# Performance work log

Measured on AMD Instinct MI355X. Metric: run time of the kernel, lower is better.

The kernel has to match this reference:

```python
import jax, jax.numpy as jnp
import numpy as np

N, E, G = 50000, 800000, 256
NODE_IN, EDGE_IN, H, L, RO, OUT = 64, 16, 128, 3, 128, 2
EPS = 1e-5


def _ln(x, g, b):
    m = jnp.mean(x, axis=-1, keepdims=True)
    v = jnp.mean((x - m) ** 2, axis=-1, keepdims=True)
    return (x - m) * jax.lax.rsqrt(v + EPS) * g + b


def setup_inputs() -> dict:
    key = jax.random.key(0)
    ks = iter(jax.random.split(key, 40))
    w = lambda *s: jax.random.normal(next(ks), s, dtype=jnp.float32) * 0.05
    inp = {
        "x": jax.random.normal(next(ks), (N, NODE_IN), dtype=jnp.float32),
        "edge_attr": jax.random.normal(next(ks), (E, EDGE_IN), dtype=jnp.float32),
        "edge_index": jax.random.randint(next(ks), (2, E), 0, N, dtype=jnp.int32),
        "batch": jnp.sort(jax.random.randint(next(ks), (N,), 0, G, dtype=jnp.int32)),
        # encoders + input norms
        "node_enc_w": w(NODE_IN, H), "node_enc_b": jnp.zeros((H,), jnp.float32),
        "edge_enc_w": w(EDGE_IN, H), "edge_enc_b": jnp.zeros((H,), jnp.float32),
        "node_ln_g": jnp.ones((H,), jnp.float32), "node_ln_b": jnp.zeros((H,), jnp.float32),
        "edge_ln_g": jnp.ones((H,), jnp.float32), "edge_ln_b": jnp.zeros((H,), jnp.float32),
        # per-layer stacked params [L, ...]
        "msg_w1": w(L, 2 * H, H), "msg_b1": jnp.zeros((L, H), jnp.float32),
        "msg_w2": w(L, H, H), "msg_b2": jnp.zeros((L, H), jnp.float32),
        "gate_w": w(L, 2 * H, H), "gate_b": jnp.zeros((L, H), jnp.float32),
        "res_w1": w(L, 2 * H, H), "res_b1": jnp.zeros((L, H), jnp.float32),
        "res_w2": w(L, H, H), "res_b2": jnp.zeros((L, H), jnp.float32),
        "ln_g": jnp.ones((L, H), jnp.float32), "ln_b": jnp.zeros((L, H), jnp.float32),
        # readout MLP
        "ro_w1": w(H, RO), "ro_b1": jnp.zeros((RO,), jnp.float32),
        "ro_w2": w(RO, OUT), "ro_b2": jnp.zeros((OUT,), jnp.float32),
    }
    return inp


def reference(x, edge_attr, edge_index, batch,
              node_enc_w, node_enc_b, edge_enc_w, edge_enc_b,
              node_ln_g, node_ln_b, edge_ln_g, edge_ln_b,
              msg_w1, msg_b1, msg_w2, msg_b2, gate_w, gate_b,
              res_w1, res_b1, res_w2, res_b2, ln_g, ln_b,
              ro_w1, ro_b1, ro_w2, ro_b2):
    src, dst = edge_index[0], edge_index[1]
    h = _ln(x @ node_enc_w + node_enc_b, node_ln_g, node_ln_b)        # [N,H]
    e = _ln(edge_attr @ edge_enc_w + edge_enc_b, edge_ln_g, edge_ln_b)  # [E,H]
    for l in range(L):
        cat = jnp.concatenate([h[src], e], axis=-1)                   # [E,2H]
        gate = jax.nn.sigmoid(cat @ gate_w[l] + gate_b[l])
        msg = jax.nn.relu(cat @ msg_w1[l] + msg_b1[l]) @ msg_w2[l] + msg_b2[l]
        agg = jax.ops.segment_sum(gate * msg, dst, num_segments=N)    # scatter-add
        comb = jnp.concatenate([h, agg], axis=-1)                     # [N,2H]
        res = jax.nn.relu(comb @ res_w1[l] + res_b1[l]) @ res_w2[l] + res_b2[l]
        h = _ln(h + res, ln_g[l], ln_b[l])
    # global mean pool over graphs
    sums = jax.ops.segment_sum(h, batch, num_segments=G)              # [G,H]
    cnt = jax.ops.segment_sum(jnp.ones((h.shape[0],), h.dtype), batch, num_segments=G)
    g = sums / jnp.maximum(cnt, 1.0)[:, None]
    return jax.nn.relu(g @ ro_w1 + ro_b1) @ ro_w2 + ro_b2             # [G,OUT]
```

## Files before the change

### kernel.cpp

```cpp
#include <hip/hip_runtime.h>
#include <math.h>

#define NN 50000
#define NE 800000
#define NG 256
#define H 128
#define NIN 64
#define EIN 16
#define NL 3
#define LEPS 1e-5f

typedef short bf16x8 __attribute__((ext_vector_type(8)));
typedef float f32x4 __attribute__((ext_vector_type(4)));
typedef float f32x16 __attribute__((ext_vector_type(16)));

__device__ __forceinline__ short bf16rne(float x) {
  unsigned u = __float_as_uint(x);
  unsigned r = u + 0x7fff + ((u >> 16) & 1);
  return (short)(r >> 16);
}

__device__ __forceinline__ float wsum(float v) {
#pragma unroll
  for (int m = 1; m < 64; m <<= 1) v += __shfl_xor(v, m, 64);
  return v;
}

__device__ __forceinline__ float lds_f32(const short* p) {
  short2 s = *(const short2*)p;
  return __uint_as_float((unsigned)(unsigned short)s.x |
                         ((unsigned)(unsigned short)s.y << 16));
}

__global__ __launch_bounds__(256) void k_count(const int* __restrict__ eidx,
                                               unsigned* __restrict__ cnt) {
  int t = blockIdx.x * 256 + threadIdx.x;
  if (t < NE) atomicAdd(&cnt[eidx[NE + t]], 1u);
}

__global__ __launch_bounds__(1024) void k_scan(const unsigned* __restrict__ cnt,
                                               unsigned* __restrict__ rowptr) {
  __shared__ unsigned part[16];
  __shared__ unsigned carry_s;
  const int tid = threadIdx.x, lane = tid & 63, wid = tid >> 6;
  if (tid == 0) carry_s = 0;
  __syncthreads();
  for (int base = 0; base < NN; base += 1024) {
    int i = base + tid;
    unsigned v = (i < NN) ? cnt[i] : 0u;
    unsigned incl = v;
#pragma unroll
    for (int off = 1; off < 64; off <<= 1) {
      unsigned t = __shfl_up(incl, off, 64);
      if (lane >= off) incl += t;
    }
    if (lane == 63) part[wid] = incl;
    __syncthreads();
    if (tid == 0) {
      unsigned s = 0;
#pragma unroll
      for (int w = 0; w < 16; w++) { unsigned t = part[w]; part[w] = s; s += t; }
    }
    __syncthreads();
    unsigned carry = carry_s;
    if (i < NN) rowptr[i] = carry + part[wid] + incl - v;
    __syncthreads();
    if (tid == 1023) carry_s = carry + part[15] + incl;
    __syncthreads();
  }
}

__global__ __launch_bounds__(256) void k_fold(
    const float* __restrict__ gate_w, const float* __restrict__ msg_w1,
    const float* __restrict__ e_enc_w, const float* __restrict__ e_enc_b,
    const float* __restrict__ e_ln_g, const float* __restrict__ e_ln_b,
    short* __restrict__ w2e, float* __restrict__ c123,
    float* __restrict__ stats) {
  const int S_W2E = 3 * 4096;
  const int S_C = S_W2E + 3 * 768;
  const int S_ST = S_C + 290;
  int tid = blockIdx.x * 256 + threadIdx.x;
  if (tid >= S_ST) return;
  if (tid < S_W2E) {
    int l = tid / 4096, e = tid % 4096;
    int t = e >> 9, lane = (e >> 3) & 63, j = e & 7;
    int k = (lane >> 5) * 8 + j;
    int n = t * 32 + (lane & 31);
    float s = 0.f;
    for (int m = 0; m < 128; m++) {
      float w = (n < 128) ? gate_w[((size_t)l * 256 + 128 + m) * 128 + n]
                          : msg_w1[((size_t)l * 256 + 128 + m) * 128 + (n - 128)];
      s += e_enc_w[k * 128 + m] * e_ln_g[m] * w;
    }
    w2e[tid] = bf16rne(s);
  } else if (tid < S_C) {
    int e = tid - S_W2E;
    int l = e / 768, r = e % 768, which = r / 256, n = r % 256;
    float s = 0.f;
    for (int m = 0; m < 128; m++) {
      float w = (n < 128) ? gate_w[((size_t)l * 256 + 128 + m) * 128 + n]
                          : msg_w1[((size_t)l * 256 + 128 + m) * 128 + (n - 128)];
      float f = (which == 0) ? e_enc_b[m] * e_ln_g[m]
              : (which == 1) ? e_ln_g[m] : e_ln_b[m];
      s += f * w;
    }
    c123[e] = s;
  } else {
    int e = tid - S_C;
    if (e < 256) {
      int i = e >> 4, j = e & 15;
      float s = 0.f;
      for (int n = 0; n < 128; n++)
        s += e_enc_w[i * 128 + n] * e_enc_w[j * 128 + n];
      stats[e] = s;
    } else if (e < 272) {
      int k = e - 256;
      float s = 0.f;
      for (int n = 0; n < 128; n++) s += e_enc_w[k * 128 + n];
      stats[e] = s;
    } else if (e < 288) {
      int k = e - 272;
      float s = 0.f;
      for (int n = 0; n < 128; n++) s += e_enc_w[k * 128 + n] * e_enc_b[n];
      stats[e] = s;
    } else if (e == 288) {
      float s = 0.f;
      for (int n = 0; n < 128; n++) s += e_enc_b[n] * e_enc_b[n];
      stats[e] = s;
    } else {
      float s = 0.f;
      for (int n = 0; n < 128; n++) s += e_enc_b[n];
      stats[e] = s;
    }
  }
}

__global__ __launch_bounds__(256) void k_scatter(
    const int* __restrict__ eidx, const float* __restrict__ ea,
    const unsigned* __restrict__ rowptr, unsigned* __restrict__ cursor,
    const float* __restrict__ stats,
    int* __restrict__ src_s, int* __restrict__ dst_s,
    short* __restrict__ ea_bf, float2* __restrict__ rsmu) {
  __shared__ float S[290];
  for (int i = threadIdx.x; i < 290; i += 256) S[i] = stats[i];
  __syncthreads();
  int t = blockIdx.x * 256 + threadIdx.x;
  int s = eidx[t], d = eidx[NE + t];
  unsigned pos = rowptr[d] + atomicAdd(&cursor[d], 1u);
  src_s[pos] = s;
  dst_s[pos] = d;
  const float4* er = (const float4*)(ea + (size_t)t * EIN);
  float4 q0 = er[0], q1 = er[1], q2 = er[2], q3 = er[3];
  float e16[16];
  e16[0]=q0.x; e16[1]=q0.y; e16[2]=q0.z; e16[3]=q0.w;
  e16[4]=q1.x; e16[5]=q1.y; e16[6]=q1.z; e16[7]=q1.w;
  e16[8]=q2.x; e16[9]=q2.y; e16[10]=q2.z; e16[11]=q2.w;
  e16[12]=q3.x; e16[13]=q3.y; e16[14]=q3.z; e16[15]=q3.w;
  short tmp[16];
#pragma unroll
  for (int j = 0; j < 16; j++) tmp[j] = bf16rne(e16[j]);
  short* dstp = ea_bf + (size_t)pos * EIN;
  *(bf16x8*)dstp = *(bf16x8*)tmp;
  *(bf16x8*)(dstp + 8) = *(bf16x8*)(tmp + 8);
  float s1 = S[289], s2 = S[288];
#pragma unroll
  for (int k = 0; k < 16; k++) {
    s1 = fmaf(e16[k], S[256 + k], s1);
    s2 = fmaf(2.f * e16[k], S[272 + k], s2);
  }
#pragma unroll
  for (int i = 0; i < 16; i++) {
    float mi = 0.f;
#pragma unroll
    for (int j = 0; j < 16; j++) mi = fmaf(S[i * 16 + j], e16[j], mi);
    s2 = fmaf(e16[i], mi, s2);
  }
  float mu = s1 * (1.f / 128.f);
  float var = s2 * (1.f / 128.f) - mu * mu;
  float rs = rsqrtf(var + LEPS);
  rsmu[pos] = make_float2(rs, mu);
}

__global__ __launch_bounds__(256) void k_convert_w(
    const float* __restrict__ gate_w, const float* __restrict__ msg_w1,
    const float* __restrict__ msg_w2, const float* __restrict__ e_enc_w,
    const float* __restrict__ res_w1, const float* __restrict__ res_w2,
    short* __restrict__ bgh, short* __restrict__ bm2, short* __restrict__ benc,
    short* __restrict__ brs1, short* __restrict__ brs2) {
  const int S_BGH = 3 * 65536;
  const int S_BM2 = S_BGH + 3 * 16384;
  const int S_BEN = S_BM2 + 2048;
  const int S_BR1 = S_BEN + 3 * 32768;
  const int S_BR2 = S_BR1 + 3 * 16384;
  int tid = blockIdx.x * 256 + threadIdx.x;
  if (tid >= S_BR2) return;
  if (tid < S_BGH) {
    int l = tid / 65536, e = tid % 65536;
    int f = e >> 9, lane = (e >> 3) & 63, j = e & 7;
    int nt = f >> 4, ks = f & 15;
    int k = ks * 16 + (lane >> 5) * 8 + j;
    int n = nt * 32 + (lane & 31);
    float v = (n < 128) ? gate_w[((size_t)l * 256 + k) * 128 + n]
                        : msg_w1[((size_t)l * 256 + k) * 128 + (n - 128)];
    bgh[tid] = bf16rne(v);
  } else if (tid < S_BM2) {
    int e0 = tid - S_BGH;
    int l = e0 / 16384, e = e0 % 16384;
    int f = e >> 9, lane = (e >> 3) & 63, j = e & 7;
    int nt = f >> 3, ks = f & 7;
    int k = ks * 16 + (lane >> 5) * 8 + j;
    int n = nt * 32 + (lane & 31);
    bm2[e0] = bf16rne(msg_w2[((size_t)l * 128 + k) * 128 + n]);
  } else if (tid < S_BEN) {
    int e = tid - S_BM2;
    int t = e >> 9, lane = (e >> 3) & 63, j = e & 7;
    int k = (lane >> 5) * 8 + j;
    int n = t * 32 + (lane & 31);
    benc[e] = bf16rne(e_enc_w[k * H + n]);
  } else if (tid < S_BR1) {
    int e0 = tid - S_BEN;
    int l = e0 / 32768, e = e0 % 32768;
    int f = e >> 9, lane = (e >> 3) & 63, j = e & 7;
    int nt = f >> 3, ks = f & 7;
    int k = ks * 32 + (lane >> 4) * 8 + j;
    int n = nt * 16 + (lane & 15);
    brs1[e0] = bf16rne(res_w1[((size_t)l * 256 + k) * 128 + n]);
  } else {
    int e0 = tid - S_BR1;
    int l = e0 / 16384, e = e0 % 16384;
    int f = e >> 9, lane = (e >> 3) & 63, j = e & 7;
    int nt = f >> 2, ks = f & 3;
    int k = ks * 32 + (lane >> 4) * 8 + j;
    int n = nt * 16 + (lane & 15);
    brs2[e0] = bf16rne(res_w2[((size_t)l * 128 + k) * 128 + n]);
  }
}

__global__ __launch_bounds__(256) void k_node_encode(
    const float* __restrict__ x, const float* __restrict__ W,
    const float* __restrict__ bias,
    const float* __restrict__ lng, const float* __restrict__ lnb,
    float* __restrict__ h, short* __restrict__ h_bf) {
  __shared__ float xs[4][8 * NIN];
  const int wave = threadIdx.x >> 6, lane = threadIdx.x & 63;
  const int n0 = (blockIdx.x * 4 + wave) * 8;
  float* xt = xs[wave];
  for (int i = lane; i < 8 * NIN; i += 64) {
    int idx = n0 * NIN + i;
    xt[i] = (idx < NN * NIN) ? x[idx] : 0.f;
  }
  __syncthreads();
  const int c0 = lane, c1 = lane + 64;
  float a0[8], a1[8];
#pragma unroll
  for (int j = 0; j < 8; j++) { a0[j] = 0.f; a1[j] = 0.f; }
  for (int k = 0; k < NIN; k++) {
    float w0 = W[k * H + c0], w1 = W[k * H + c1];
#pragma unroll
    for (int j = 0; j < 8; j++) {
      float xv = xt[j * NIN + k];
      a0[j] = fmaf(xv, w0, a0[j]);
      a1[j] = fmaf(xv, w1, a1[j]);
    }
  }
  const float b0 = bias[c0], b1 = bias[c1];
  const float g0 = lng[c0], g1 = lng[c1], lb0 = lnb[c0], lb1 = lnb[c1];
#pragma unroll
  for (int j = 0; j < 8; j++) {
    float v0 = a0[j] + b0, v1 = a1[j] + b1;
    float mean = wsum(v0 + v1) * (1.f / H);
    float d0 = v0 - mean, d1 = v1 - mean;
    float var = wsum(d0 * d0 + d1 * d1) * (1.f / H);
    float rs = rsqrtf(var + LEPS);
    int n = n0 + j;
    if (n < NN) {
      float o0 = d0 * rs * g0 + lb0, o1 = d1 * rs * g1 + lb1;
      h[n * H + c0] = o0;
      h[n * H + c1] = o1;
      h_bf[n * H + c0] = bf16rne(o0);
      h_bf[n * H + c1] = bf16rne(o1);
    }
  }
}

__global__ __launch_bounds__(256) void k_edge_mfma(
    const short* __restrict__ ea_bf, const float2* __restrict__ rsmu,
    const int* __restrict__ src_s, const int* __restrict__ dst_s,
    const short* __restrict__ h_bf,
    const short* __restrict__ Bgh, const short* __restrict__ Bm2,
    const short* __restrict__ W2e, const float* __restrict__ c123,
    const float* __restrict__ gbias, const float* __restrict__ mbias1,
    const float* __restrict__ mbias2,
    float* __restrict__ agg) {
  __shared__ short regn[4][32 * 136];
  __shared__ int dsts[4][32];
  __shared__ float rsS[4][32], muS[4][32];
  const int tid = threadIdx.x;
  const int wave = tid >> 6, lane = tid & 63;
  const int e0 = blockIdx.x * 128 + wave * 32;
  short* R = regn[wave];
  const int c31 = lane & 31, halfl = lane >> 5;
  const int koff = halfl * 8;

  if (lane < 32) {
    dsts[wave][lane] = dst_s[e0 + lane];
    float2 rm = rsmu[e0 + lane];
    rsS[wave][lane] = rm.x;
    muS[wave][lane] = rm.y;
  }

  const int srow = src_s[e0 + c31];
  bf16x8 af[8];
#pragma unroll
  for (int ks = 0; ks < 8; ks++)
    af[ks] = *(const bf16x8*)(h_bf + (size_t)srow * H + ks * 16 + koff);

  const float rs_own = rsmu[e0 + c31].x;
  bf16x8 ae;
  {
    bf16x8 raw = *(const bf16x8*)(ea_bf + (size_t)(e0 + c31) * EIN + koff);
#pragma unroll
    for (int j = 0; j < 8; j++) {
      float f = __uint_as_float(((unsigned)(unsigned short)raw[j]) << 16);
      ae[j] = bf16rne(f * rs_own);
    }
  }

  float rsR[16], rmR[16];
#pragma unroll
  for (int r = 0; r < 16; r++) {
    int row = (r & 3) + 8 * (r >> 2) + 4 * halfl;
    rsR[r] = rsS[wave][row];
    rmR[r] = rsR[r] * muS[wave][row];
  }

#pragma unroll
  for (int ht = 0; ht < 4; ht++) {
    const int nt = 4 + ht;
    f32x16 a = __builtin_amdgcn_mfma_f32_32x32x16_bf16(
        ae, *(const bf16x8*)(W2e + (size_t)(nt * 64 + lane) * 8),
        (f32x16)(0.f), 0, 0, 0);
#pragma unroll
    for (int ks = 0; ks < 8; ks++) {
      bf16x8 bf = *(const bf16x8*)(Bgh + (size_t)((nt * 16 + ks) * 64 + lane) * 8);
      a = __builtin_amdgcn_mfma_f32_32x32x16_bf16(af[ks], bf, a, 0, 0, 0);
    }
    const int col = ht * 32 + c31;
    const int n = nt * 32 + c31;
    const float c1v = c123[n], c2v = c123[256 + n];
    const float c3b = c123[512 + n] + mbias1[col];
#pragma unroll
    for (int r = 0; r < 16; r++) {
      int row = (r & 3) + 8 * (r >> 2) + 4 * halfl;
      float pre = fmaf(rsR[r], c1v, fmaf(-rmR[r], c2v, a[r] + c3b));
      R[row * 136 + col] = bf16rne(fmaxf(pre, 0.f));
    }
  }

  float gate[4][16];
#pragma unroll
  for (int gt = 0; gt < 4; gt++) {
    f32x16 a = __builtin_amdgcn_mfma_f32_32x32x16_bf16(
        ae, *(const bf16x8*)(W2e + (size_t)(gt * 64 + lane) * 8),
        (f32x16)(0.f), 0, 0, 0);
#pragma unroll
    for (int ks = 0; ks < 8; ks++) {
      bf16x8 bf = *(const bf16x8*)(Bgh + (size_t)((gt * 16 + ks) * 64 + lane) * 8);
      a = __builtin_amdgcn_mfma_f32_32x32x16_bf16(af[ks], bf, a, 0, 0, 0);
    }
    const int n = gt * 32 + c31;
    const float c1v = c123[n], c2v = c123[256 + n];
    const float c3b = c123[512 + n] + gbias[n];
#pragma unroll
    for (int r = 0; r < 16; r++) {
      float pre = fmaf(rsR[r], c1v, fmaf(-rmR[r], c2v, a[r] + c3b));
      gate[gt][r] = __builtin_amdgcn_rcpf(1.f + __expf(-pre));
    }
  }

  bf16x8 a2[8];
#pragma unroll
  for (int ks = 0; ks < 8; ks++)
    a2[ks] = *(const bf16x8*)&R[c31 * 136 + ks * 16 + koff];

#pragma unroll
  for (int halfM = 0; halfM < 2; halfM++) {
#pragma unroll
    for (int t2 = 0; t2 < 2; t2++) {
      int gt = halfM * 2 + t2;
      f32x16 m = (f32x16)(0.f);
#pragma unroll
      for (int ks = 0; ks < 8; ks++) {
        bf16x8 bf = *(const bf16x8*)(Bm2 + (size_t)((gt * 8 + ks) * 64 + lane) * 8);
        m = __builtin_amdgcn_mfma_f32_32x32x16_bf16(a2[ks], bf, m, 0, 0, 0);
      }
      float mb2 = mbias2[gt * 32 + c31];
      int c2 = t2 * 32 + c31;
#pragma unroll
      for (int r = 0; r < 16; r++) {
        int row = (r & 3) + 8 * (r >> 2) + 4 * halfl;
        float msg = gate[gt][r] * (m[r] + mb2);
        unsigned u = __float_as_uint(msg);
        *(short2*)&R[row * 136 + c2 * 2] =
            make_short2((short)(u & 0xffff), (short)(u >> 16));
      }
    }
    const int colg = halfM * 64 + lane;
    int cur = dsts[wave][0];
    float run = lds_f32(&R[lane * 2]);
#pragma unroll
    for (int row = 1; row < 32; row++) {
      int d = dsts[wave][row];
      float v = lds_f32(&R[row * 136 + lane * 2]);
      if (d == cur) {
        run += v;
      } else {
        atomicAdd(&agg[(size_t)cur * H + colg], run);
        cur = d; run = v;
      }
    }
    atomicAdd(&agg[(size_t)cur * H + colg], run);
  }
}

__global__ __launch_bounds__(256) void k_node_up2(
    float* agg, const short* __restrict__ h_bf_in,
    const float* __restrict__ h_in,
    const short* __restrict__ Brs1, const short* __restrict__ Brs2,
    const float* __restrict__ rb1, const float* __restrict__ rb2,
    const float* __restrict__ lng, const float* __restrict__ lnb,
    float* __restrict__ h, short* __restrict__ h_bf) {
  __shared__ short regn[4][16 * 136];
  const int tid = threadIdx.x;
  const int wave = tid >> 6, lane = tid & 63;
  const int n0 = blockIdx.x * 64 + wave * 16;
  short* R = regn[wave];
  const int mrow = lane & 15, quad = lane >> 4;

  int nr = n0 + mrow; if (nr >= NN) nr = NN - 1;
  bf16x8 af[8];
#pragma unroll
  for (int ks = 0; ks < 4; ks++)
    af[ks] = *(const bf16x8*)(h_bf_in + (size_t)nr * H + ks * 32 + quad * 8);
#pragma unroll
  for (int ks = 0; ks < 4; ks++) {
    float4 u = *(const float4*)(agg + (size_t)nr * H + ks * 32 + quad * 8);
    float4 w = *(const float4*)(agg + (size_t)nr * H + ks * 32 + quad * 8 + 4);
    short tmp[8];
    tmp[0]=bf16rne(u.x); tmp[1]=bf16rne(u.y); tmp[2]=bf16rne(u.z); tmp[3]=bf16rne(u.w);
    tmp[4]=bf16rne(w.x); tmp[5]=bf16rne(w.y); tmp[6]=bf16rne(w.z); tmp[7]=bf16rne(w.w);
    af[4 + ks] = *(bf16x8*)tmp;
  }
  float4 z4 = make_float4(0.f, 0.f, 0.f, 0.f);
#pragma unroll
  for (int ks = 0; ks < 4; ks++) {
    *(float4*)(agg + (size_t)nr * H + ks * 32 + quad * 8) = z4;
    *(float4*)(agg + (size_t)nr * H + ks * 32 + quad * 8 + 4) = z4;
  }

#pragma unroll
  for (int t = 0; t < 8; t++) {
    f32x4 a = (f32x4){0.f, 0.f, 0.f, 0.f};
#pragma unroll
    for (int ks = 0; ks < 8; ks++) {
      bf16x8 bf = *(const bf16x8*)(Brs1 + (size_t)((t * 8 + ks) * 64 + lane) * 8);
      a = __builtin_amdgcn_mfma_f32_16x16x32_bf16(af[ks], bf, a, 0, 0, 0);
    }
    int col = t * 16 + mrow;
    float b = rb1[col];
#pragma unroll
    for (int r = 0; r < 4; r++)
      R[(quad * 4 + r) * 136 + col] = bf16rne(fmaxf(a[r] + b, 0.f));
  }
  bf16x8 a2[4];
#pragma unroll
  for (int ks = 0; ks < 4; ks++)
    a2[ks] = *(const bf16x8*)&R[mrow * 136 + ks * 32 + quad * 8];

  float vals[8][4];
  float gl[8], bl[8];
#pragma unroll
  for (int t = 0; t < 8; t++) {
    f32x4 a = (f32x4){0.f, 0.f, 0.f, 0.f};
#pragma unroll
    for (int ks = 0; ks < 4; ks++) {
      bf16x8 bf = *(const bf16x8*)(Brs2 + (size_t)((t * 4 + ks) * 64 + lane) * 8);
      a = __builtin_amdgcn_mfma_f32_16x16x32_bf16(a2[ks], bf, a, 0, 0, 0);
    }
    int col = t * 16 + mrow;
    float b2 = rb2[col];
    gl[t] = lng[col]; bl[t] = lnb[col];
#pragma unroll
    for (int r = 0; r < 4; r++) {
      int rowi = n0 + quad * 4 + r;
      int rl = rowi < NN ? rowi : NN - 1;
      vals[t][r] = h_in[(size_t)rl * H + col] + a[r] + b2;
    }
  }
#pragma unroll
  for (int r = 0; r < 4; r++) {
    float s1 = 0.f, s2 = 0.f;
#pragma unroll
    for (int t = 0; t < 8; t++) {
      s1 += vals[t][r];
      s2 = fmaf(vals[t][r], vals[t][r], s2);
    }
#pragma unroll
    for (int m = 1; m < 16; m <<= 1) {
      s1 += __shfl_xor(s1, m, 64);
      s2 += __shfl_xor(s2, m, 64);
    }
    float mean = s1 * (1.f / 128.f);
    float var = s2 * (1.f / 128.f) - mean * mean;
    float rs = rsqrtf(var + LEPS);
    int rowi = n0 + quad * 4 + r;
    if (rowi < NN) {
#pragma unroll
      for (int t = 0; t < 8; t++) {
        int col = t * 16 + mrow;
        float o = (vals[t][r] - mean) * rs * gl[t] + bl[t];
        h[(size_t)rowi * H + col] = o;
        h_bf[(size_t)rowi * H + col] = bf16rne(o);
      }
    }
  }
}

__global__ __launch_bounds__(256) void k_pool(
    const float* __restrict__ h, const int* __restrict__ batch,
    float* __restrict__ gsum, float* __restrict__ gcnt) {
  const int tid = threadIdx.x;
  const int col = tid & 127, half = tid >> 7;
  int n0 = blockIdx.x * 32 + half * 16;
  if (n0 >= NN) return;
  int end = n0 + 16; if (end > NN) end = NN;
  int cur = batch[n0];
  float run = h[(size_t)n0 * H + col];
  float cnt = 1.f;
  for (int n = n0 + 1; n < end; n++) {
    int b = batch[n];
    float v = h[(size_t)n * H + col];
    if (b == cur) { run += v; cnt += 1.f; }
    else {
      atomicAdd(&gsum[(size_t)cur * H + col], run);
      if (col == 0) atomicAdd(&gcnt[cur], cnt);
      cur = b; run = v; cnt = 1.f;
    }
  }
  atomicAdd(&gsum[(size_t)cur * H + col], run);
  if (col == 0) atomicAdd(&gcnt[cur], cnt);
}

__global__ __launch_bounds__(128) void k_readout(
    const float* __restrict__ gsum, const float* __restrict__ gcnt,
    const float* __restrict__ W1, const float* __restrict__ b1,
    const float* __restrict__ W2, const float* __restrict__ b2,
    float* __restrict__ out) {
  __shared__ float gs[H];
  __shared__ float o1[H];
  int b = blockIdx.x, c = threadIdx.x;
  float cnt = fmaxf(gcnt[b], 1.f);
  gs[c] = gsum[b * H + c] / cnt;
  __syncthreads();
  float acc = b1[c];
  for (int k = 0; k < H; k++) acc = fmaf(gs[k], W1[k * H + c], acc);
  o1[c] = fmaxf(acc, 0.f);
  __syncthreads();
  if (c < 2) {
    float acc2 = b2[c];
    for (int k = 0; k < H; k++) acc2 = fmaf(o1[k], W2[k * 2 + c], acc2);
    out[b * 2 + c] = acc2;
  }
}

extern "C" void kernel_launch(void* const* d_in, const int* in_sizes, int n_in,
                              void* d_out, int out_size, void* d_ws, size_t ws_size,
                              hipStream_t stream) {
  (void)in_sizes; (void)n_in; (void)out_size; (void)ws_size;
  const float* x       = (const float*)d_in[0];
  const float* ea      = (const float*)d_in[1];
  const int*   eidx    = (const int*)d_in[2];
  const int*   batch   = (const int*)d_in[3];
  const float* n_enc_w = (const float*)d_in[4];
  const float* n_enc_b = (const float*)d_in[5];
  const float* e_enc_w = (const float*)d_in[6];
  const float* e_enc_b = (const float*)d_in[7];
  const float* n_ln_g  = (const float*)d_in[8];
  const float* n_ln_b  = (const float*)d_in[9];
  const float* e_ln_g  = (const float*)d_in[10];
  const float* e_ln_b  = (const float*)d_in[11];
  const float* msg_w1  = (const float*)d_in[12];
  const float* msg_b1  = (const float*)d_in[13];
  const float* msg_w2  = (const float*)d_in[14];
  const float* msg_b2  = (const float*)d_in[15];
  const float* gate_w  = (const float*)d_in[16];
  const float* gate_b  = (const float*)d_in[17];
  const float* res_w1  = (const float*)d_in[18];
  const float* res_b1  = (const float*)d_in[19];
  const float* res_w2  = (const float*)d_in[20];
  const float* res_b2  = (const float*)d_in[21];
  const float* ln_g    = (const float*)d_in[22];
  const float* ln_b    = (const float*)d_in[23];
  const float* ro_w1   = (const float*)d_in[24];
  const float* ro_b1   = (const float*)d_in[25];
  const float* ro_w2   = (const float*)d_in[26];
  const float* ro_b2   = (const float*)d_in[27];

  char* p = (char*)d_ws;
  float* h     = (float*)p;  p += (size_t)NN * H * 4;
  short* h_bf  = (short*)p;  p += (size_t)NN * H * 2;
  float* agg   = (float*)p;  p += (size_t)NN * H * 4;
  short* ea_bf = (short*)p;  p += (size_t)NE * EIN * 2;
  float2* rsmu = (float2*)p; p += (size_t)NE * 8;
  float* gsum  = (float*)p;  p += (size_t)NG * H * 4;
  float* gcnt  = (float*)p;  p += 1024;
  short* bgh   = (short*)p;  p += (size_t)3 * 65536 * 2;
  short* bm2   = (short*)p;  p += (size_t)3 * 16384 * 2;
  short* benc  = (short*)p;  p += (size_t)2048 * 2;
  short* brs1  = (short*)p;  p += (size_t)3 * 32768 * 2;
  short* brs2  = (short*)p;  p += (size_t)3 * 16384 * 2;
  short* w2e   = (short*)p;  p += (size_t)3 * 4096 * 2;
  float* c123  = (float*)p;  p += (size_t)3 * 768 * 4;
  float* stats = (float*)p;  p += 2048;
  unsigned* rowptr = (unsigned*)p; p += ((size_t)NN * 4 + 15) / 16 * 16;
  unsigned* cursor = (unsigned*)p; p += ((size_t)NN * 4 + 15) / 16 * 16;
  int* src_s   = (int*)p;    p += (size_t)NE * 4;
  int* dst_s   = (int*)p;    p += (size_t)NE * 4;

  const int node_blocks = (NN + 31) / 32;
  const int nup_blocks  = (NN + 63) / 64;
  const int edge_blocks = NE / 128;
  const int e256 = (NE + 255) / 256;
  const int conv_total = 3 * 65536 + 3 * 16384 + 2048 + 3 * 32768 + 3 * 16384;
  const int fold_total = 3 * 4096 + 3 * 768 + 290;

  hipMemsetAsync(cursor, 0, (size_t)NN * 4, stream);
  k_fold<<<(fold_total + 255) / 256, 256, 0, stream>>>(
      gate_w, msg_w1, e_enc_w, e_enc_b, e_ln_g, e_ln_b, w2e, c123, stats);
  k_count<<<e256, 256, 0, stream>>>(eidx, cursor);
  k_scan<<<1, 1024, 0, stream>>>(cursor, rowptr);
  hipMemsetAsync(cursor, 0, (size_t)NN * 4, stream);
  k_scatter<<<e256, 256, 0, stream>>>(eidx, ea, rowptr, cursor, stats,
                                      src_s, dst_s, ea_bf, rsmu);

  k_convert_w<<<(conv_total + 255) / 256, 256, 0, stream>>>(
      gate_w, msg_w1, msg_w2, e_enc_w, res_w1, res_w2,
      bgh, bm2, benc, brs1, brs2);
  k_node_encode<<<node_blocks, 256, 0, stream>>>(x, n_enc_w, n_enc_b, n_ln_g, n_ln_b, h, h_bf);

  hipMemsetAsync(agg, 0, (size_t)NN * H * 4, stream);
  for (int l = 0; l < NL; l++) {
    k_edge_mfma<<<edge_blocks, 256, 0, stream>>>(
        ea_bf, rsmu, src_s, dst_s, h_bf,
        bgh + (size_t)l * 65536, bm2 + (size_t)l * 16384,
        w2e + (size_t)l * 4096, c123 + (size_t)l * 768,
        gate_b + l * H, msg_b1 + l * H, msg_b2 + l * H, agg);
    k_node_up2<<<nup_blocks, 256, 0, stream>>>(
        agg, h_bf, h,
        brs1 + (size_t)l * 32768, brs2 + (size_t)l * 16384,
        res_b1 + l * H, res_b2 + l * H,
        ln_g + l * H, ln_b + l * H, h, h_bf);
  }

  hipMemsetAsync(gsum, 0, ((size_t)NG * H + NG) * 4, stream);
  k_pool<<<(NN + 31) / 32, 256, 0, stream>>>(h, batch, gsum, gcnt);
  k_readout<<<NG, 128, 0, stream>>>(gsum, gcnt, ro_w1, ro_b1, ro_w2, ro_b2, (float*)d_out);
}
```

Measured before the change: 1.023 ms.

## Fold edge LN correction and biases into extra MFMA K-steps, transpose edge tiles

The per-edge layernorm correction terms (rs, -rs*mu, constant) and the gate/msg1/msg2 biases are folded into extra K columns of the weight fragments, so the edge kernel applies them with one or two additional MFMAs instead of scalar epilogue FMAs and c123 loads. The MFMA operands are swapped so the accumulator comes out transposed. This lets the ReLU'd hidden activations be repacked into the next A operand with lane shuffles instead of a round trip through shared memory. The message output is staged as fp32 in shared memory for the segmented reduction, and bf16 packing now uses the paired conversion intrinsic. Risks are extra bf16 rounding on the folded bias and correction terms and extra MFMA work.

```diff
diff --git a/kernel.cpp b/kernel.cpp
--- a/kernel.cpp
+++ b/kernel.cpp
@@ -1,4 +1,5 @@
 #include <hip/hip_runtime.h>
+#include <hip/hip_bf16.h>
 #include <math.h>
 
 #define NN 50000
@@ -13,6 +14,7 @@
 typedef short bf16x8 __attribute__((ext_vector_type(8)));
 typedef float f32x4 __attribute__((ext_vector_type(4)));
 typedef float f32x16 __attribute__((ext_vector_type(16)));
+typedef unsigned u32x4 __attribute__((ext_vector_type(4)));
 
 __device__ __forceinline__ short bf16rne(float x) {
   unsigned u = __float_as_uint(x);
@@ -20,16 +22,15 @@
   return (short)(r >> 16);
 }
 
+__device__ __forceinline__ unsigned pk2(float lo, float hi) {
+  __hip_bfloat162 h = __float22bfloat162_rn(make_float2(lo, hi));
+  return *(unsigned*)&h;
+}
+
 __device__ __forceinline__ float wsum(float v) {
 #pragma unroll
   for (int m = 1; m < 64; m <<= 1) v += __shfl_xor(v, m, 64);
   return v;
-}
-
-__device__ __forceinline__ float lds_f32(const short* p) {
-  short2 s = *(const short2*)p;
-  return __uint_as_float((unsigned)(unsigned short)s.x |
-                         ((unsigned)(unsigned short)s.y << 16));
 }
 
 __global__ __launch_bounds__(256) void k_count(const int* __restrict__ eidx,
@@ -72,41 +73,37 @@
 
 __global__ __launch_bounds__(256) void k_fold(
     const float* __restrict__ gate_w, const float* __restrict__ msg_w1,
+    const float* __restrict__ gate_b, const float* __restrict__ msg_b1,
     const float* __restrict__ e_enc_w, const float* __restrict__ e_enc_b,
     const float* __restrict__ e_ln_g, const float* __restrict__ e_ln_b,
-    short* __restrict__ w2e, float* __restrict__ c123,
-    float* __restrict__ stats) {
-  const int S_W2E = 3 * 4096;
-  const int S_C = S_W2E + 3 * 768;
-  const int S_ST = S_C + 290;
+    short* __restrict__ w2e, float* __restrict__ stats) {
+  const int S_W2E = 3 * 8192;
+  const int S_ST = S_W2E + 290;
   int tid = blockIdx.x * 256 + threadIdx.x;
   if (tid >= S_ST) return;
   if (tid < S_W2E) {
-    int l = tid / 4096, e = tid % 4096;
-    int t = e >> 9, lane = (e >> 3) & 63, j = e & 7;
-    int k = (lane >> 5) * 8 + j;
-    int n = t * 32 + (lane & 31);
+    int l = tid / 8192, e = tid % 8192;
+    int f = e >> 9, lane = (e >> 3) & 63, j = e & 7;
+    int nt = f >> 1, ks2 = f & 1;
+    int k = ks2 * 16 + (lane >> 5) * 8 + j;
+    int n = nt * 32 + (lane & 31);
     float s = 0.f;
-    for (int m = 0; m < 128; m++) {
-      float w = (n < 128) ? gate_w[((size_t)l * 256 + 128 + m) * 128 + n]
-                          : msg_w1[((size_t)l * 256 + 128 + m) * 128 + (n - 128)];
-      s += e_enc_w[k * 128 + m] * e_ln_g[m] * w;
+    if (k < 19) {
+      for (int m = 0; m < 128; m++) {
+        float w = (n < 128) ? gate_w[((size_t)l * 256 + 128 + m) * 128 + n]
+                            : msg_w1[((size_t)l * 256 + 128 + m) * 128 + (n - 128)];
+        float fm = (k < 16)   ? e_enc_w[k * 128 + m] * e_ln_g[m]
+                 : (k == 16)  ? e_enc_b[m] * e_ln_g[m]
+                 : (k == 17)  ? e_ln_g[m]
+                              : e_ln_b[m];
+        s += fm * w;
+      }
+      if (k == 18)
+        s += (n < 128) ? gate_b[l * 128 + n] : msg_b1[l * 128 + (n - 128)];
     }
     w2e[tid] = bf16rne(s);
-  } else if (tid < S_C) {
+  } else {
     int e = tid - S_W2E;
-    int l = e / 768, r = e % 768, which = r / 256, n = r % 256;
-    float s = 0.f;
-    for (int m = 0; m < 128; m++) {
-      float w = (n < 128) ? gate_w[((size_t)l * 256 + 128 + m) * 128 + n]
-                          : msg_w1[((size_t)l * 256 + 128 + m) * 128 + (n - 128)];
-      float f = (which == 0) ? e_enc_b[m] * e_ln_g[m]
-              : (which == 1) ? e_ln_g[m] : e_ln_b[m];
-      s += f * w;
-    }
-    c123[e] = s;
-  } else {
-    int e = tid - S_C;
     if (e < 256) {
       int i = e >> 4, j = e & 15;
       float s = 0.f;
@@ -156,12 +153,12 @@
   e16[4]=q1.x; e16[5]=q1.y; e16[6]=q1.z; e16[7]=q1.w;
   e16[8]=q2.x; e16[9]=q2.y; e16[10]=q2.z; e16[11]=q2.w;
   e16[12]=q3.x; e16[13]=q3.y; e16[14]=q3.z; e16[15]=q3.w;
-  short tmp[16];
-#pragma unroll
-  for (int j = 0; j < 16; j++) tmp[j] = bf16rne(e16[j]);
-  short* dstp = ea_bf + (size_t)pos * EIN;
-  *(bf16x8*)dstp = *(bf16x8*)tmp;
-  *(bf16x8*)(dstp + 8) = *(bf16x8*)(tmp + 8);
+  unsigned pk[8];
+#pragma unroll
+  for (int j = 0; j < 8; j++) pk[j] = pk2(e16[2 * j], e16[2 * j + 1]);
+  unsigned* dstp = (unsigned*)(ea_bf + (size_t)pos * EIN);
+#pragma unroll
+  for (int j = 0; j < 8; j++) dstp[j] = pk[j];
   float s1 = S[289], s2 = S[288];
 #pragma unroll
   for (int k = 0; k < 16; k++) {
@@ -183,14 +180,13 @@
 
 __global__ __launch_bounds__(256) void k_convert_w(
     const float* __restrict__ gate_w, const float* __restrict__ msg_w1,
-    const float* __restrict__ msg_w2, const float* __restrict__ e_enc_w,
+    const float* __restrict__ msg_w2, const float* __restrict__ msg_b2,
     const float* __restrict__ res_w1, const float* __restrict__ res_w2,
-    short* __restrict__ bgh, short* __restrict__ bm2, short* __restrict__ benc,
+    short* __restrict__ bgh, short* __restrict__ bm2,
     short* __restrict__ brs1, short* __restrict__ brs2) {
   const int S_BGH = 3 * 65536;
-  const int S_BM2 = S_BGH + 3 * 16384;
-  const int S_BEN = S_BM2 + 2048;
-  const int S_BR1 = S_BEN + 3 * 32768;
+  const int S_BM2 = S_BGH + 3 * 18432;
+  const int S_BR1 = S_BM2 + 3 * 32768;
   const int S_BR2 = S_BR1 + 3 * 16384;
   int tid = blockIdx.x * 256 + threadIdx.x;
   if (tid >= S_BR2) return;
@@ -205,20 +201,20 @@
     bgh[tid] = bf16rne(v);
   } else if (tid < S_BM2) {
     int e0 = tid - S_BGH;
-    int l = e0 / 16384, e = e0 % 16384;
+    int l = e0 / 18432, e = e0 % 18432;
     int f = e >> 9, lane = (e >> 3) & 63, j = e & 7;
-    int nt = f >> 3, ks = f & 7;
-    int k = ks * 16 + (lane >> 5) * 8 + j;
-    int n = nt * 32 + (lane & 31);
-    bm2[e0] = bf16rne(msg_w2[((size_t)l * 128 + k) * 128 + n]);
-  } else if (tid < S_BEN) {
-    int e = tid - S_BM2;
-    int t = e >> 9, lane = (e >> 3) & 63, j = e & 7;
-    int k = (lane >> 5) * 8 + j;
-    int n = t * 32 + (lane & 31);
-    benc[e] = bf16rne(e_enc_w[k * H + n]);
+    int gt = f / 9, ks = f % 9;
+    int n = gt * 32 + (lane & 31);
+    float v;
+    if (ks < 8) {
+      int k = ks * 16 + (lane >> 5) * 8 + j;
+      v = msg_w2[((size_t)l * 128 + k) * 128 + n];
+    } else {
+      v = ((lane >> 5) == 0 && j == 0) ? msg_b2[l * 128 + n] : 0.f;
+    }
+    bm2[e0] = bf16rne(v);
   } else if (tid < S_BR1) {
-    int e0 = tid - S_BEN;
+    int e0 = tid - S_BM2;
     int l = e0 / 32768, e = e0 % 32768;
     int f = e >> 9, lane = (e >> 3) & 63, j = e & 7;
     int nt = f >> 3, ks = f & 7;
@@ -287,27 +283,18 @@
     const short* __restrict__ ea_bf, const float2* __restrict__ rsmu,
     const int* __restrict__ src_s, const int* __restrict__ dst_s,
     const short* __restrict__ h_bf,
-    const short* __restrict__ Bgh, const short* __restrict__ Bm2,
-    const short* __restrict__ W2e, const float* __restrict__ c123,
-    const float* __restrict__ gbias, const float* __restrict__ mbias1,
-    const float* __restrict__ mbias2,
-    float* __restrict__ agg) {
-  __shared__ short regn[4][32 * 136];
+    const short* __restrict__ Bgh, const short* __restrict__ Bm2x,
+    const short* __restrict__ W2e, float* __restrict__ agg) {
+  __shared__ float regn[4][32 * 68];
   __shared__ int dsts[4][32];
-  __shared__ float rsS[4][32], muS[4][32];
   const int tid = threadIdx.x;
   const int wave = tid >> 6, lane = tid & 63;
   const int e0 = blockIdx.x * 128 + wave * 32;
-  short* R = regn[wave];
+  float* R = regn[wave];
   const int c31 = lane & 31, halfl = lane >> 5;
   const int koff = halfl * 8;
 
-  if (lane < 32) {
-    dsts[wave][lane] = dst_s[e0 + lane];
-    float2 rm = rsmu[e0 + lane];
-    rsS[wave][lane] = rm.x;
-    muS[wave][lane] = rm.y;
-  }
+  if (lane < 32) dsts[wave][lane] = dst_s[e0 + lane];
 
   const int srow = src_s[e0 + c31];
   bf16x8 af[8];
@@ -315,103 +302,123 @@
   for (int ks = 0; ks < 8; ks++)
     af[ks] = *(const bf16x8*)(h_bf + (size_t)srow * H + ks * 16 + koff);
 
-  const float rs_own = rsmu[e0 + c31].x;
+  const float2 rm = rsmu[e0 + c31];
   bf16x8 ae;
   {
     bf16x8 raw = *(const bf16x8*)(ea_bf + (size_t)(e0 + c31) * EIN + koff);
-#pragma unroll
-    for (int j = 0; j < 8; j++) {
-      float f = __uint_as_float(((unsigned)(unsigned short)raw[j]) << 16);
-      ae[j] = bf16rne(f * rs_own);
-    }
-  }
-
-  float rsR[16], rmR[16];
-#pragma unroll
-  for (int r = 0; r < 16; r++) {
-    int row = (r & 3) + 8 * (r >> 2) + 4 * halfl;
-    rsR[r] = rsS[wave][row];
-    rmR[r] = rsR[r] * muS[wave][row];
-  }
-
+    u32x4 v;
+#pragma unroll
+    for (int p = 0; p < 4; p++) {
+      float lo = __uint_as_float(((unsigned)(unsigned short)raw[2 * p]) << 16) * rm.x;
+      float hi = __uint_as_float(((unsigned)(unsigned short)raw[2 * p + 1]) << 16) * rm.x;
+      v[p] = pk2(lo, hi);
+    }
+    ae = __builtin_bit_cast(bf16x8, v);
+  }
+  bf16x8 ae2;
+  {
+    u32x4 v;
+    v[0] = halfl ? 0u : pk2(rm.x, -rm.x * rm.y);
+    v[1] = halfl ? 0u : 0x00003F80u;
+    v[2] = 0u; v[3] = 0u;
+    ae2 = __builtin_bit_cast(bf16x8, v);
+  }
+  bf16x8 onefrag;
+  {
+    u32x4 v;
+    v[0] = halfl ? 0u : 0x00003F80u;
+    v[1] = 0u; v[2] = 0u; v[3] = 0u;
+    onefrag = __builtin_bit_cast(bf16x8, v);
+  }
+
+  u32x4 a2v[8];
 #pragma unroll
   for (int ht = 0; ht < 4; ht++) {
     const int nt = 4 + ht;
     f32x16 a = __builtin_amdgcn_mfma_f32_32x32x16_bf16(
-        ae, *(const bf16x8*)(W2e + (size_t)(nt * 64 + lane) * 8),
+        *(const bf16x8*)(W2e + (size_t)((nt * 2 + 0) * 64 + lane) * 8), ae,
         (f32x16)(0.f), 0, 0, 0);
-#pragma unroll
-    for (int ks = 0; ks < 8; ks++) {
-      bf16x8 bf = *(const bf16x8*)(Bgh + (size_t)((nt * 16 + ks) * 64 + lane) * 8);
-      a = __builtin_amdgcn_mfma_f32_32x32x16_bf16(af[ks], bf, a, 0, 0, 0);
-    }
-    const int col = ht * 32 + c31;
-    const int n = nt * 32 + c31;
-    const float c1v = c123[n], c2v = c123[256 + n];
-    const float c3b = c123[512 + n] + mbias1[col];
-#pragma unroll
-    for (int r = 0; r < 16; r++) {
-      int row = (r & 3) + 8 * (r >> 2) + 4 * halfl;
-      float pre = fmaf(rsR[r], c1v, fmaf(-rmR[r], c2v, a[r] + c3b));
-      R[row * 136 + col] = bf16rne(fmaxf(pre, 0.f));
-    }
-  }
-
-  float gate[4][16];
-#pragma unroll
-  for (int gt = 0; gt < 4; gt++) {
-    f32x16 a = __builtin_amdgcn_mfma_f32_32x32x16_bf16(
-        ae, *(const bf16x8*)(W2e + (size_t)(gt * 64 + lane) * 8),
-        (f32x16)(0.f), 0, 0, 0);
-#pragma unroll
-    for (int ks = 0; ks < 8; ks++) {
-      bf16x8 bf = *(const bf16x8*)(Bgh + (size_t)((gt * 16 + ks) * 64 + lane) * 8);
-      a = __builtin_amdgcn_mfma_f32_32x32x16_bf16(af[ks], bf, a, 0, 0, 0);
-    }
-    const int n = gt * 32 + c31;
-    const float c1v = c123[n], c2v = c123[256 + n];
-    const float c3b = c123[512 + n] + gbias[n];
-#pragma unroll
-    for (int r = 0; r < 16; r++) {
-      float pre = fmaf(rsR[r], c1v, fmaf(-rmR[r], c2v, a[r] + c3b));
-      gate[gt][r] = __builtin_amdgcn_rcpf(1.f + __expf(-pre));
-    }
-  }
-
-  bf16x8 a2[8];
-#pragma unroll
-  for (int ks = 0; ks < 8; ks++)
-    a2[ks] = *(const bf16x8*)&R[c31 * 136 + ks * 16 + koff];
+    a = __builtin_amdgcn_mfma_f32_32x32x16_bf16(
+        *(const bf16x8*)(W2e + (size_t)((nt * 2 + 1) * 64 + lane) * 8), ae2,
+        a, 0, 0, 0);
+#pragma unroll
+    for (int ks = 0; ks < 8; ks++)
+      a = __builtin_amdgcn_mfma_f32_32x32x16_bf16(
+          *(const bf16x8*)(Bgh + (size_t)((nt * 16 + ks) * 64 + lane) * 8),
+          af[ks], a, 0, 0, 0);
+    unsigned q[8];
+#pragma unroll
+    for (int qq = 0; qq < 4; qq++) {
+      q[2 * qq]     = pk2(fmaxf(a[4 * qq], 0.f),     fmaxf(a[4 * qq + 1], 0.f));
+      q[2 * qq + 1] = pk2(fmaxf(a[4 * qq + 2], 0.f), fmaxf(a[4 * qq + 3], 0.f));
+    }
+    unsigned x0a = __shfl_xor(halfl ? q[0] : q[2], 32, 64);
+    unsigned x0b = __shfl_xor(halfl ? q[1] : q[3], 32, 64);
+    unsigned x1a = __shfl_xor(halfl ? q[4] : q[6], 32, 64);
+    unsigned x1b = __shfl_xor(halfl ? q[5] : q[7], 32, 64);
+    u32x4 F0, F1;
+    F0[0] = halfl ? x0a : q[0];
+    F0[1] = halfl ? x0b : q[1];
+    F0[2] = halfl ? q[2] : x0a;
+    F0[3] = halfl ? q[3] : x0b;
+    F1[0] = halfl ? x1a : q[4];
+    F1[1] = halfl ? x1b : q[5];
+    F1[2] = halfl ? q[6] : x1a;
+    F1[3] = halfl ? q[7] : x1b;
+    a2v[2 * ht] = F0;
+    a2v[2 * ht + 1] = F1;
+  }
 
 #pragma unroll
   for (int halfM = 0; halfM < 2; halfM++) {
+    float gate[2][16];
 #pragma unroll
     for (int t2 = 0; t2 < 2; t2++) {
-      int gt = halfM * 2 + t2;
+      const int gt = halfM * 2 + t2;
+      f32x16 a = __builtin_amdgcn_mfma_f32_32x32x16_bf16(
+          *(const bf16x8*)(W2e + (size_t)((gt * 2 + 0) * 64 + lane) * 8), ae,
+          (f32x16)(0.f), 0, 0, 0);
+      a = __builtin_amdgcn_mfma_f32_32x32x16_bf16(
+          *(const bf16x8*)(W2e + (size_t)((gt * 2 + 1) * 64 + lane) * 8), ae2,
+          a, 0, 0, 0);
+#pragma unroll
+      for (int ks = 0; ks < 8; ks++)
+        a = __builtin_amdgcn_mfma_f32_32x32x16_bf16(
+            *(const bf16x8*)(Bgh + (size_t)((gt * 16 + ks) * 64 + lane) * 8),
+            af[ks], a, 0, 0, 0);
+#pragma unroll
+      for (int r = 0; r < 16; r++)
+        gate[t2][r] = __builtin_amdgcn_rcpf(1.f + __expf(-a[r]));
+    }
+#pragma unroll
+    for (int t2 = 0; t2 < 2; t2++) {
+      const int gt = halfM * 2 + t2;
       f32x16 m = (f32x16)(0.f);
 #pragma unroll
-      for (int ks = 0; ks < 8; ks++) {
-        bf16x8 bf = *(const bf16x8*)(Bm2 + (size_t)((gt * 8 + ks) * 64 + lane) * 8);
-        m = __builtin_amdgcn_mfma_f32_32x32x16_bf16(a2[ks], bf, m, 0, 0, 0);
-      }
-      float mb2 = mbias2[gt * 32 + c31];
-      int c2 = t2 * 32 + c31;
-#pragma unroll
-      for (int r = 0; r < 16; r++) {
-        int row = (r & 3) + 8 * (r >> 2) + 4 * halfl;
-        float msg = gate[gt][r] * (m[r] + mb2);
-        unsigned u = __float_as_uint(msg);
-        *(short2*)&R[row * 136 + c2 * 2] =
-            make_short2((short)(u & 0xffff), (short)(u >> 16));
+      for (int ks = 0; ks < 8; ks++)
+        m = __builtin_amdgcn_mfma_f32_32x32x16_bf16(
+            *(const bf16x8*)(Bm2x + (size_t)((gt * 9 + ks) * 64 + lane) * 8),
+            __builtin_bit_cast(bf16x8, a2v[ks]), m, 0, 0, 0);
+      m = __builtin_amdgcn_mfma_f32_32x32x16_bf16(
+          *(const bf16x8*)(Bm2x + (size_t)((gt * 9 + 8) * 64 + lane) * 8),
+          onefrag, m, 0, 0, 0);
+#pragma unroll
+      for (int qq = 0; qq < 4; qq++) {
+        f32x4 mv;
+        mv[0] = gate[t2][4 * qq] * m[4 * qq];
+        mv[1] = gate[t2][4 * qq + 1] * m[4 * qq + 1];
+        mv[2] = gate[t2][4 * qq + 2] * m[4 * qq + 2];
+        mv[3] = gate[t2][4 * qq + 3] * m[4 * qq + 3];
+        *(f32x4*)&R[c31 * 68 + t2 * 32 + qq * 8 + halfl * 4] = mv;
       }
     }
     const int colg = halfM * 64 + lane;
     int cur = dsts[wave][0];
-    float run = lds_f32(&R[lane * 2]);
+    float run = R[lane];
 #pragma unroll
     for (int row = 1; row < 32; row++) {
       int d = dsts[wave][row];
-      float v = lds_f32(&R[row * 136 + lane * 2]);
+      float v = R[row * 68 + lane];
       if (d == cur) {
         run += v;
       } else {
@@ -446,10 +453,10 @@
   for (int ks = 0; ks < 4; ks++) {
     float4 u = *(const float4*)(agg + (size_t)nr * H + ks * 32 + quad * 8);
     float4 w = *(const float4*)(agg + (size_t)nr * H + ks * 32 + quad * 8 + 4);
-    short tmp[8];
-    tmp[0]=bf16rne(u.x); tmp[1]=bf16rne(u.y); tmp[2]=bf16rne(u.z); tmp[3]=bf16rne(u.w);
-    tmp[4]=bf16rne(w.x); tmp[5]=bf16rne(w.y); tmp[6]=bf16rne(w.z); tmp[7]=bf16rne(w.w);
-    af[4 + ks] = *(bf16x8*)tmp;
+    u32x4 v;
+    v[0] = pk2(u.x, u.y); v[1] = pk2(u.z, u.w);
+    v[2] = pk2(w.x, w.y); v[3] = pk2(w.z, w.w);
+    af[4 + ks] = __builtin_bit_cast(bf16x8, v);
   }
   float4 z4 = make_float4(0.f, 0.f, 0.f, 0.f);
 #pragma unroll
@@ -615,12 +622,10 @@
   float* gsum  = (float*)p;  p += (size_t)NG * H * 4;
   float* gcnt  = (float*)p;  p += 1024;
   short* bgh   = (short*)p;  p += (size_t)3 * 65536 * 2;
-  short* bm2   = (short*)p;  p += (size_t)3 * 16384 * 2;
-  short* benc  = (short*)p;  p += (size_t)2048 * 2;
+  short* bm2   = (short*)p;  p += (size_t)3 * 18432 * 2;
   short* brs1  = (short*)p;  p += (size_t)3 * 32768 * 2;
   short* brs2  = (short*)p;  p += (size_t)3 * 16384 * 2;
-  short* w2e   = (short*)p;  p += (size_t)3 * 4096 * 2;
-  float* c123  = (float*)p;  p += (size_t)3 * 768 * 4;
+  short* w2e   = (short*)p;  p += (size_t)3 * 8192 * 2;
   float* stats = (float*)p;  p += 2048;
   unsigned* rowptr = (unsigned*)p; p += ((size_t)NN * 4 + 15) / 16 * 16;
   unsigned* cursor = (unsigned*)p; p += ((size_t)NN * 4 + 15) / 16 * 16;
@@ -631,12 +636,13 @@
   const int nup_blocks  = (NN + 63) / 64;
   const int edge_blocks = NE / 128;
   const int e256 = (NE + 255) / 256;
-  const int conv_total = 3 * 65536 + 3 * 16384 + 2048 + 3 * 32768 + 3 * 16384;
-  const int fold_total = 3 * 4096 + 3 * 768 + 290;
+  const int conv_total = 3 * 65536 + 3 * 18432 + 3 * 32768 + 3 * 16384;
+  const int fold_total = 3 * 8192 + 290;
 
   hipMemsetAsync(cursor, 0, (size_t)NN * 4, stream);
   k_fold<<<(fold_total + 255) / 256, 256, 0, stream>>>(
-      gate_w, msg_w1, e_enc_w, e_enc_b, e_ln_g, e_ln_b, w2e, c123, stats);
+      gate_w, msg_w1, gate_b, msg_b1, e_enc_w, e_enc_b, e_ln_g, e_ln_b,
+      w2e, stats);
   k_count<<<e256, 256, 0, stream>>>(eidx, cursor);
   k_scan<<<1, 1024, 0, stream>>>(cursor, rowptr);
   hipMemsetAsync(cursor, 0, (size_t)NN * 4, stream);
@@ -644,17 +650,16 @@
                                       src_s, dst_s, ea_bf, rsmu);
 
   k_convert_w<<<(conv_total + 255) / 256, 256, 0, stream>>>(
-      gate_w, msg_w1, msg_w2, e_enc_w, res_w1, res_w2,
-      bgh, bm2, benc, brs1, brs2);
+      gate_w, msg_w1, msg_w2, msg_b2, res_w1, res_w2,
+      bgh, bm2, brs1, brs2);
   k_node_encode<<<node_blocks, 256, 0, stream>>>(x, n_enc_w, n_enc_b, n_ln_g, n_ln_b, h, h_bf);
 
   hipMemsetAsync(agg, 0, (size_t)NN * H * 4, stream);
   for (int l = 0; l < NL; l++) {
     k_edge_mfma<<<edge_blocks, 256, 0, stream>>>(
         ea_bf, rsmu, src_s, dst_s, h_bf,
-        bgh + (size_t)l * 65536, bm2 + (size_t)l * 16384,
-        w2e + (size_t)l * 4096, c123 + (size_t)l * 768,
-        gate_b + l * H, msg_b1 + l * H, msg_b2 + l * H, agg);
+        bgh + (size_t)l * 65536, bm2 + (size_t)l * 18432,
+        w2e + (size_t)l * 8192, agg);
     k_node_up2<<<nup_blocks, 256, 0, stream>>>(
         agg, h_bf, h,
         brs1 + (size_t)l * 32768, brs2 + (size_t)l * 16384,
```

After: 1.300 ms. +27.0%, slower.
